# Performance work log

Measured on AMD Instinct MI355X. Metric: run time of the kernel, lower is better.

## Reference

```python
import jax, jax.numpy as jnp
import numpy as np

KERNEL = 3  # kernel_size from init_kwargs


def _unfold(x, k):
    """torch.nn.functional.unfold with padding=k//2, stride=1.
    Returns [b, c*k*k, h*w] with torch's ordering: index = c*(k*k) + kh*k + kw.
    """
    b, c, h, w = x.shape
    p = k // 2
    xp = jnp.pad(x, ((0, 0), (0, 0), (p, p), (p, p)))
    # fixed k*k = 9 slices (small static loop, not a data-dim loop)
    cols = jnp.stack(
        [xp[:, :, i:i + h, j:j + w] for i in range(k) for j in range(k)],
        axis=2,
    )  # [b, c, k*k, h, w]
    return cols.reshape(b, c * k * k, h * w)


def setup_inputs() -> dict:
    key = jax.random.key(0)
    k1, k2 = jax.random.split(key)
    x = jax.random.normal(k1, (8, 64, 128, 128), dtype=jnp.float32)
    # memory parameter: torch.rand -> uniform [0, 1), shape [c*k*k, out_channels]
    memory = jax.random.uniform(k2, (64 * KERNEL * KERNEL, 128), dtype=jnp.float32)
    return {"x": x, "memory": memory}


def reference(x, memory):
    b, c, h, w = x.shape
    cols = _unfold(x, KERNEL)                 # [b, c*k*k, h*w]
    cols = jax.nn.softmax(cols, axis=1)       # softmax over unfolded patch dim
    out = jnp.einsum('ki,bkl->bil', memory, cols)  # [b, out_ch, h*w]
    return out.reshape(b, memory.shape[1], h, w)
```

## Files before the change

### kernel.cpp

```cpp
#include <hip/hip_runtime.h>
#include <stdint.h>


#define Cn 64
#define Hn 128
#define Wn 128
#define OC 128
#define HW (Hn * Wn)

typedef __attribute__((ext_vector_type(8))) short bf16x8_t;
typedef __attribute__((ext_vector_type(16))) float f32x16_t;

__device__ inline unsigned short f2bf(float f) {
    union { float f; uint32_t u; } v; v.f = f;
    uint32_t u = v.u;
    u += 0x7fffu + ((u >> 16) & 1u);
    return (unsigned short)(u >> 16);
}
__device__ inline float bf_lo(uint32_t u) {
    union { uint32_t u; float f; } v; v.u = u << 16;
    return v.f;
}
__device__ inline float bf_hi(uint32_t u) {
    union { uint32_t u; float f; } v; v.u = u & 0xffff0000u;
    return v.f;
}

__global__ void prep_b2(const float* __restrict__ mem, uint4* __restrict__ Bt2) {
    int u = blockIdx.x * 256 + threadIdx.x;
    int n = u & 127;
    int cid = u >> 7;
    int hi = cid & 1;
    int kc = cid >> 1;
    int q = kc >> 2, cblk = kc & 3;
    unsigned short h8[8];
#pragma unroll
    for (int j = 0; j < 8; j++) {
        int c = cblk * 16 + hi * 8 + j;
        h8[j] = f2bf(mem[(c * 9 + q) * OC + n]);
    }
    Bt2[cid * 128 + n] = *(const uint4*)h8;
}

__global__ __launch_bounds__(256, 4) void convf(const float* __restrict__ x,
                                                const uint4* __restrict__ Bt2,
                                                float* __restrict__ out) {
    __shared__ __align__(16) uint4 EtL[108 * 8];
    __shared__ float Sh[108];

    int bid0 = blockIdx.x;
    int bid = ((bid0 & 7) << 8) | (bid0 >> 3);
    int b = bid >> 8;
    int ty = (bid >> 3) & 31, tx = bid & 7;
    int h0 = ty * 4, w0 = tx * 16;
    int t = threadIdx.x;
    int lane = t & 63;

    const float* xb = x + (size_t)b * Cn * HW;

#pragma unroll
    for (int it = 0; it < 2; it++) {
        int u = it * 256 + t;
        if (u < 288) {
            int g = u & 7;
            int pg = u >> 3;
            int py = pg / 6, qs = pg % 6;
            int gy = h0 - 1 + py;
            bool inrow = (gy >= 0) & (gy < Hn);

            if (qs >= 1 && qs <= 4) {
                int px0 = (qs - 1) * 4 + 1;
                float4 v[8];
                if (inrow) {
                    const float* basep = xb + (size_t)(8 * g) * HW
                                       + (size_t)gy * Wn + (w0 + (qs - 1) * 4);
#pragma unroll
                    for (int k = 0; k < 8; k++)
                        v[k] = *(const float4*)(basep + (size_t)k * HW);
                }
                float s4[4];
#pragma unroll
                for (int i = 0; i < 4; i++) {
                    uint32_t wd[4];
                    float si;
                    if (inrow) {
                        si = 0.f;
#pragma unroll
                        for (int j = 0; j < 4; j++) {
                            float a = ((const float*)&v[2 * j])[i];
                            float c = ((const float*)&v[2 * j + 1])[i];
                            uint32_t pk = (uint32_t)f2bf(__expf(a))
                                        | ((uint32_t)f2bf(__expf(c)) << 16);
                            wd[j] = pk;
                            si += bf_lo(pk) + bf_hi(pk);
                        }
                    } else {
                        wd[0] = wd[1] = wd[2] = wd[3] = 0x3F803F80u;
                        si = 8.f;
                    }
                    int p = py * 18 + px0 + i;
                    EtL[p * 8 + (g ^ (p & 7))] = *(const uint4*)wd;
                    s4[i] = si;
                }
#pragma unroll
                for (int m = 1; m < 8; m <<= 1) {
#pragma unroll
                    for (int i = 0; i < 4; i++)
                        s4[i] += __shfl_xor(s4[i], m);
                }
                if (g < 4) Sh[py * 18 + px0 + g] = s4[g];
            } else {
                int side = (qs == 5);
                int p = py * 18 + (side ? 17 : 0);
                int gxe = side ? (w0 + 16) : (w0 - 1);
                bool real = inrow && (gxe >= 0) && (gxe < Wn);
                uint32_t wd[4];
                float s;
                if (real) {
                    const float* basep = xb + (size_t)(8 * g) * HW
                                       + (size_t)gy * Wn + gxe;
                    s = 0.f;
#pragma unroll
                    for (int j = 0; j < 4; j++) {
                        float a = basep[(size_t)(2 * j) * HW];
                        float c = basep[(size_t)(2 * j + 1) * HW];
                        uint32_t pk = (uint32_t)f2bf(__expf(a))
                                    | ((uint32_t)f2bf(__expf(c)) << 16);
                        wd[j] = pk;
                        s += bf_lo(pk) + bf_hi(pk);
                    }
                } else {
                    wd[0] = wd[1] = wd[2] = wd[3] = 0x3F803F80u;
                    s = 8.f;
                }
                EtL[p * 8 + (g ^ (p & 7))] = *(const uint4*)wd;
#pragma unroll
                for (int m = 1; m < 8; m <<= 1)
                    s += __shfl_xor(s, m);
                if (g == 0) Sh[p] = s;
            }
        }
    }
    __syncthreads();

    int wo = t >> 6;
    int l31 = lane & 31, hi = lane >> 5;
    int x0v = l31 & 15;
    int y0[2];
    y0[0] = 0 + (l31 >> 4);
    y0[1] = 2 + (l31 >> 4);

    f32x16_t acc[2];
#pragma unroll
    for (int j = 0; j < 2; j++)
#pragma unroll
        for (int r = 0; r < 16; r++) acc[j][r] = 0.f;

    bf16x8_t Wf[4], Ef[4][2];

    auto loadW = [&](int kc, int s) {
        Wf[s] = *(const bf16x8_t*)(Bt2 + (size_t)((kc * 2 + hi) * 128 + wo * 32 + l31));
    };
    auto loadE = [&](int kc, int s) {
        int q = kc >> 2, cblk = kc & 3;
        int kh = q / 3, kw = q - kh * 3;
        int ge = cblk * 2 + hi;
#pragma unroll
        for (int j = 0; j < 2; j++) {
            int pix = (y0[j] + kh) * 18 + (x0v + kw);
            Ef[s][j] = *(const bf16x8_t*)&EtL[pix * 8 + (ge ^ (pix & 7))];
        }
    };

    loadW(0, 0); loadE(0, 0);
    loadW(1, 1); loadE(1, 1);
    loadW(2, 2); loadE(2, 2);
    loadW(3, 3); loadE(3, 3);
#pragma unroll
    for (int kc = 0; kc < 36; kc++) {
        int s = kc & 3;
#pragma unroll
        for (int j = 0; j < 2; j++)
            acc[j] = __builtin_amdgcn_mfma_f32_32x32x16_bf16(
                Wf[s], Ef[s][j], acc[j], 0, 0, 0);
        if (kc + 4 < 36) { loadW(kc + 4, s); loadE(kc + 4, s); }
    }

#pragma unroll
    for (int j = 0; j < 2; j++) {
        float z = 0.f;
#pragma unroll
        for (int dy = 0; dy < 3; dy++)
#pragma unroll
            for (int dx = 0; dx < 3; dx++)
                z += Sh[(y0[j] + dy) * 18 + (x0v + dx)];
        float zi = 1.0f / z;
        float* ob = out + (size_t)b * OC * HW + (size_t)(wo * 32 + 4 * hi) * HW
                  + (h0 + y0[j]) * Wn + (w0 + x0v);
#pragma unroll
        for (int r = 0; r < 16; r++) {
            int nrel = (r & 3) + 8 * (r >> 2);
            ob[(size_t)nrel * HW] = acc[j][r] * zi;
        }
    }
}

extern "C" void kernel_launch(void* const* d_in, const int* in_sizes, int n_in,
                              void* d_out, int out_size, void* d_ws, size_t ws_size,
                              hipStream_t stream) {
    const float* x = (const float*)d_in[0];
    const float* mem = (const float*)d_in[1];
    float* out = (float*)d_out;

    uint4* Bt2 = (uint4*)d_ws;

    prep_b2<<<36, 256, 0, stream>>>(mem, Bt2);
    convf<<<2048, 256, 0, stream>>>(x, Bt2, out);
}
```

Baseline: 135.4 us.

## Double spatial tile height to 8 rows with 512-thread blocks and rebalance prefetch

Each block now covers an 8x16 output tile with 8 waves (4 output-channel groups times 2 row pairs) instead of a 4x16 tile with 4 waves. This cuts the share of halo rows whose exp/bf16 conversion is recomputed, from 6 staged rows per 4 output rows to 10 per 8. The weight-fragment prefetch depth rises to 6 and is issued before the staging phase, LDS prefetch drops to 3, and s_setprio raises wave priority around the MFMA issue. In exchange the blocks are larger with more LDS, the grid is halved, and occupancy may shift, along with register pressure from the deeper weight buffer.

```diff
diff --git a/kernel.cpp b/kernel.cpp
--- a/kernel.cpp
+++ b/kernel.cpp
@@ -42,125 +42,124 @@
     Bt2[cid * 128 + n] = *(const uint4*)h8;
 }
 
-__global__ __launch_bounds__(256, 4) void convf(const float* __restrict__ x,
+__global__ __launch_bounds__(512, 4) void convf(const float* __restrict__ x,
                                                 const uint4* __restrict__ Bt2,
                                                 float* __restrict__ out) {
-    __shared__ __align__(16) uint4 EtL[108 * 8];
-    __shared__ float Sh[108];
+    __shared__ __align__(16) uint4 EtL[180 * 8];
+    __shared__ float Sh[180];
 
     int bid0 = blockIdx.x;
-    int bid = ((bid0 & 7) << 8) | (bid0 >> 3);
-    int b = bid >> 8;
-    int ty = (bid >> 3) & 31, tx = bid & 7;
-    int h0 = ty * 4, w0 = tx * 16;
+    int bid = ((bid0 & 7) << 7) | (bid0 >> 3);
+    int b = bid >> 7;
+    int ty = (bid >> 3) & 15, tx = bid & 7;
+    int h0 = ty * 8, w0 = tx * 16;
     int t = threadIdx.x;
-    int lane = t & 63;
+    int lane = t & 63, wid = t >> 6;
+
+    int wo = wid & 3;
+    int wp = wid >> 2;
+    int l31 = lane & 31, hi = lane >> 5;
+    int x0v = l31 & 15;
+    int y0[2];
+    y0[0] = (wp * 2 + 0) * 2 + (l31 >> 4);
+    y0[1] = (wp * 2 + 1) * 2 + (l31 >> 4);
+
+    bf16x8_t Wf[6], Ef[3][2];
+    auto loadW = [&](int kc, int s) {
+        Wf[s] = *(const bf16x8_t*)(Bt2 + (size_t)((kc * 2 + hi) * 128 + wo * 32 + l31));
+    };
+    loadW(0, 0); loadW(1, 1); loadW(2, 2);
+    loadW(3, 3); loadW(4, 4); loadW(5, 5);
 
     const float* xb = x + (size_t)b * Cn * HW;
 
-#pragma unroll
-    for (int it = 0; it < 2; it++) {
-        int u = it * 256 + t;
-        if (u < 288) {
-            int g = u & 7;
-            int pg = u >> 3;
-            int py = pg / 6, qs = pg % 6;
-            int gy = h0 - 1 + py;
-            bool inrow = (gy >= 0) & (gy < Hn);
-
-            if (qs >= 1 && qs <= 4) {
-                int px0 = (qs - 1) * 4 + 1;
-                float4 v[8];
+    if (t < 480) {
+        int g = t & 7;
+        int pg = t >> 3;
+        int py = pg / 6, qs = pg % 6;
+        int gy = h0 - 1 + py;
+        bool inrow = (gy >= 0) & (gy < Hn);
+
+        if (qs >= 1 && qs <= 4) {
+            int px0 = (qs - 1) * 4 + 1;
+            float4 v[8];
+            if (inrow) {
+                const float* basep = xb + (size_t)(8 * g) * HW
+                                   + (size_t)gy * Wn + (w0 + (qs - 1) * 4);
+#pragma unroll
+                for (int k = 0; k < 8; k++)
+                    v[k] = *(const float4*)(basep + (size_t)k * HW);
+            }
+            float s4[4];
+#pragma unroll
+            for (int i = 0; i < 4; i++) {
+                uint32_t wd[4];
+                float si;
                 if (inrow) {
-                    const float* basep = xb + (size_t)(8 * g) * HW
-                                       + (size_t)gy * Wn + (w0 + (qs - 1) * 4);
-#pragma unroll
-                    for (int k = 0; k < 8; k++)
-                        v[k] = *(const float4*)(basep + (size_t)k * HW);
-                }
-                float s4[4];
-#pragma unroll
-                for (int i = 0; i < 4; i++) {
-                    uint32_t wd[4];
-                    float si;
-                    if (inrow) {
-                        si = 0.f;
-#pragma unroll
-                        for (int j = 0; j < 4; j++) {
-                            float a = ((const float*)&v[2 * j])[i];
-                            float c = ((const float*)&v[2 * j + 1])[i];
-                            uint32_t pk = (uint32_t)f2bf(__expf(a))
-                                        | ((uint32_t)f2bf(__expf(c)) << 16);
-                            wd[j] = pk;
-                            si += bf_lo(pk) + bf_hi(pk);
-                        }
-                    } else {
-                        wd[0] = wd[1] = wd[2] = wd[3] = 0x3F803F80u;
-                        si = 8.f;
-                    }
-                    int p = py * 18 + px0 + i;
-                    EtL[p * 8 + (g ^ (p & 7))] = *(const uint4*)wd;
-                    s4[i] = si;
-                }
-#pragma unroll
-                for (int m = 1; m < 8; m <<= 1) {
-#pragma unroll
-                    for (int i = 0; i < 4; i++)
-                        s4[i] += __shfl_xor(s4[i], m);
-                }
-                if (g < 4) Sh[py * 18 + px0 + g] = s4[g];
-            } else {
-                int side = (qs == 5);
-                int p = py * 18 + (side ? 17 : 0);
-                int gxe = side ? (w0 + 16) : (w0 - 1);
-                bool real = inrow && (gxe >= 0) && (gxe < Wn);
-                uint32_t wd[4];
-                float s;
-                if (real) {
-                    const float* basep = xb + (size_t)(8 * g) * HW
-                                       + (size_t)gy * Wn + gxe;
-                    s = 0.f;
+                    si = 0.f;
 #pragma unroll
                     for (int j = 0; j < 4; j++) {
-                        float a = basep[(size_t)(2 * j) * HW];
-                        float c = basep[(size_t)(2 * j + 1) * HW];
+                        float a = ((const float*)&v[2 * j])[i];
+                        float c = ((const float*)&v[2 * j + 1])[i];
                         uint32_t pk = (uint32_t)f2bf(__expf(a))
                                     | ((uint32_t)f2bf(__expf(c)) << 16);
                         wd[j] = pk;
-                        s += bf_lo(pk) + bf_hi(pk);
+                        si += bf_lo(pk) + bf_hi(pk);
                     }
                 } else {
                     wd[0] = wd[1] = wd[2] = wd[3] = 0x3F803F80u;
-                    s = 8.f;
+                    si = 8.f;
                 }
+                int p = py * 18 + px0 + i;
                 EtL[p * 8 + (g ^ (p & 7))] = *(const uint4*)wd;
-#pragma unroll
-                for (int m = 1; m < 8; m <<= 1)
-                    s += __shfl_xor(s, m);
-                if (g == 0) Sh[p] = s;
-            }
+                s4[i] = si;
+            }
+#pragma unroll
+            for (int m = 1; m < 8; m <<= 1) {
+#pragma unroll
+                for (int i = 0; i < 4; i++)
+                    s4[i] += __shfl_xor(s4[i], m);
+            }
+            if (g < 4) Sh[py * 18 + px0 + g] = s4[g];
+        } else {
+            int side = (qs == 5);
+            int p = py * 18 + (side ? 17 : 0);
+            int gxe = side ? (w0 + 16) : (w0 - 1);
+            bool real = inrow && (gxe >= 0) && (gxe < Wn);
+            uint32_t wd[4];
+            float s;
+            if (real) {
+                const float* basep = xb + (size_t)(8 * g) * HW
+                                   + (size_t)gy * Wn + gxe;
+                s = 0.f;
+#pragma unroll
+                for (int j = 0; j < 4; j++) {
+                    float a = basep[(size_t)(2 * j) * HW];
+                    float c = basep[(size_t)(2 * j + 1) * HW];
+                    uint32_t pk = (uint32_t)f2bf(__expf(a))
+                                | ((uint32_t)f2bf(__expf(c)) << 16);
+                    wd[j] = pk;
+                    s += bf_lo(pk) + bf_hi(pk);
+                }
+            } else {
+                wd[0] = wd[1] = wd[2] = wd[3] = 0x3F803F80u;
+                s = 8.f;
+            }
+            EtL[p * 8 + (g ^ (p & 7))] = *(const uint4*)wd;
+#pragma unroll
+            for (int m = 1; m < 8; m <<= 1)
+                s += __shfl_xor(s, m);
+            if (g == 0) Sh[p] = s;
         }
     }
     __syncthreads();
 
-    int wo = t >> 6;
-    int l31 = lane & 31, hi = lane >> 5;
-    int x0v = l31 & 15;
-    int y0[2];
-    y0[0] = 0 + (l31 >> 4);
-    y0[1] = 2 + (l31 >> 4);
-
     f32x16_t acc[2];
 #pragma unroll
     for (int j = 0; j < 2; j++)
 #pragma unroll
         for (int r = 0; r < 16; r++) acc[j][r] = 0.f;
 
-    bf16x8_t Wf[4], Ef[4][2];
-
-    auto loadW = [&](int kc, int s) {
-        Wf[s] = *(const bf16x8_t*)(Bt2 + (size_t)((kc * 2 + hi) * 128 + wo * 32 + l31));
-    };
     auto loadE = [&](int kc, int s) {
         int q = kc >> 2, cblk = kc & 3;
         int kh = q / 3, kw = q - kh * 3;
@@ -172,18 +171,18 @@
         }
     };
 
-    loadW(0, 0); loadE(0, 0);
-    loadW(1, 1); loadE(1, 1);
-    loadW(2, 2); loadE(2, 2);
-    loadW(3, 3); loadE(3, 3);
+    loadE(0, 0); loadE(1, 1); loadE(2, 2);
 #pragma unroll
     for (int kc = 0; kc < 36; kc++) {
-        int s = kc & 3;
+        int sE = kc % 3, sW = kc % 6;
+        __builtin_amdgcn_s_setprio(1);
 #pragma unroll
         for (int j = 0; j < 2; j++)
             acc[j] = __builtin_amdgcn_mfma_f32_32x32x16_bf16(
-                Wf[s], Ef[s][j], acc[j], 0, 0, 0);
-        if (kc + 4 < 36) { loadW(kc + 4, s); loadE(kc + 4, s); }
+                Wf[sW], Ef[sE][j], acc[j], 0, 0, 0);
+        __builtin_amdgcn_s_setprio(0);
+        if (kc + 3 < 36) loadE(kc + 3, sE);
+        if (kc + 6 < 36) loadW(kc + 6, sW);
     }
 
 #pragma unroll
@@ -215,5 +214,5 @@
     uint4* Bt2 = (uint4*)d_ws;
 
     prep_b2<<<36, 256, 0, stream>>>(mem, Bt2);
-    convf<<<2048, 256, 0, stream>>>(x, Bt2, out);
-}
+    convf<<<1024, 512, 0, stream>>>(x, Bt2, out);
+}
```

Result: faster. 120.1 us (-11.4%).
